# Kernel optimization log

Hardware: AMD Instinct MI355X
Metric: run time of the kernel (lower is better)

Reference implementation:

```python
import jax, jax.numpy as jnp
import numpy as np

B, T, M, H, E = 4, 2048, 1024, 16, 8
S = B * T              # total tokens
C = S // E             # deepspeed top-1 capacity, capacity_factor = 1.0
D = M // H             # head dim


def setup_inputs() -> dict:
    key = jax.random.key(0)
    ks = jax.random.split(key, 8)
    def nrm(k, shape, scale=0.02):
        return jax.random.normal(k, shape, jnp.float32) * scale
    return {
        "x": jax.random.normal(ks[0], (B, T, M), jnp.float32),
        "ln1_g": jnp.ones((M,), jnp.float32), "ln1_b": jnp.zeros((M,), jnp.float32),
        "in_proj_w": nrm(ks[1], (3 * M, M)), "in_proj_b": jnp.zeros((3 * M,), jnp.float32),
        "out_proj_w": nrm(ks[2], (M, M)), "out_proj_b": jnp.zeros((M,), jnp.float32),
        "ln2_g": jnp.ones((M,), jnp.float32), "ln2_b": jnp.zeros((M,), jnp.float32),
        "wg": nrm(ks[3], (M, E)),
        "w1": nrm(ks[4], (E, M, 4 * M)), "b1": jnp.zeros((E, 4 * M), jnp.float32),
        "w2": nrm(ks[5], (E, 4 * M, M)), "b2": jnp.zeros((E, M), jnp.float32),
    }


def layernorm(x, g, b):
    mu = x.mean(-1, keepdims=True)
    var = x.var(-1, keepdims=True)
    return (x - mu) * jax.lax.rsqrt(var + 1e-5) * g + b


def reference(x, ln1_g, ln1_b, in_proj_w, in_proj_b, out_proj_w, out_proj_b,
              ln2_g, ln2_b, wg, w1, b1, w2, b2):
    # --- pre-norm causal self-attention (nn.MultiheadAttention, batch_first) ---
    h = layernorm(x, ln1_g, ln1_b)
    qkv = h @ in_proj_w.T + in_proj_b                 # [B,T,3M]
    q, k, v = jnp.split(qkv, 3, axis=-1)
    split_heads = lambda t: t.reshape(B, T, H, D).transpose(0, 2, 1, 3)
    q, k, v = split_heads(q), split_heads(k), split_heads(v)
    scores = jnp.einsum('bhqd,bhkd->bhqk', q, k) / np.float32(np.sqrt(D))
    causal = jnp.tril(jnp.ones((T, T), bool))
    scores = jnp.where(causal, scores, jnp.float32(-jnp.inf))
    attn = jax.nn.softmax(scores, axis=-1)
    o = jnp.einsum('bhqk,bhkd->bhqd', attn, v).transpose(0, 2, 1, 3).reshape(B, T, M)
    x = x + o @ out_proj_w.T + out_proj_b

    # --- pre-norm top-1 MoE FFN (deepspeed-style dispatch with capacity drop) ---
    h = layernorm(x, ln2_g, ln2_b)
    flat = h.reshape(S, M)
    gates = jax.nn.softmax(flat @ wg, axis=-1)        # [S,E]
    idx = jnp.argmax(gates, axis=-1)                  # top-1 expert per token
    onehot = jax.nn.one_hot(idx, E, dtype=flat.dtype) # [S,E]
    # position of each token within its expert's queue
    pos = jnp.take_along_axis(jnp.cumsum(onehot, 0) - 1.0, idx[:, None], 1)[:, 0].astype(jnp.int32)
    keep = (pos < C).astype(flat.dtype)               # capacity drop
    pos_c = jnp.clip(pos, 0, C - 1)
    gate_val = jnp.take_along_axis(gates, idx[:, None], 1)[:, 0] * keep
    # scatter-dispatch tokens -> [E,C,M]
    disp = jnp.zeros((E, C, M), flat.dtype).at[idx, pos_c].add(flat * keep[:, None])
    # per-expert grouped GEMM FFN: M -> 4M -> M with exact GELU
    h1 = jax.nn.gelu(jnp.einsum('ecm,emf->ecf', disp, w1) + b1[:, None, :], approximate=False)
    eo = jnp.einsum('ecf,efm->ecm', h1, w2) + b2[:, None, :]
    # gather-combine, weight by gate prob (dropped tokens get zero)
    moe = eo[idx, pos_c] * gate_val[:, None]
    return x + moe.reshape(B, T, M)
```

## Files before the change

kernel.cpp:

```cpp
#include <hip/hip_runtime.h>
#include <hip/hip_bf16.h>
#include <math.h>

#define B_ 4
#define T_ 2048
#define M_ 1024
#define H_ 16
#define E_ 8
#define S_ (B_*T_)
#define C_ (S_/E_)
#define D_ (M_/H_)
#define F_ (4*M_)

typedef unsigned short ushort_t;
typedef __attribute__((ext_vector_type(8))) short bf16x8;
typedef __attribute__((ext_vector_type(4))) float f32x4;

__device__ __forceinline__ float gelu_exact(float x) {
    return 0.5f * x * (1.0f + erff(x * 0.70710678118654752440f));
}

__device__ __forceinline__ unsigned short f2bf(float f) {
    unsigned int u = __float_as_uint(f);
    u = (u + 0x7FFFu + ((u >> 16) & 1u)) >> 16;
    return (unsigned short)u;
}

__device__ __forceinline__ float bf2f(unsigned short h) {
    return __uint_as_float(((unsigned)h) << 16);
}

__device__ __forceinline__ void gload_lds16(const void* g, void* l) {
    __builtin_amdgcn_global_load_lds(
        (const __attribute__((address_space(1))) unsigned int*)g,
        (__attribute__((address_space(3))) unsigned int*)l,
        16, 0, 0);
}

__device__ __forceinline__ void lgkm0() {
    asm volatile("s_waitcnt lgkmcnt(0)" ::: "memory");
}

__global__ __launch_bounds__(256) void ln_kernel(const float* __restrict__ x,
                                                 const float* __restrict__ g,
                                                 const float* __restrict__ bta,
                                                 float* __restrict__ out)
{
    const int row = blockIdx.x;
    const int tid = threadIdx.x;
    const float4 v = reinterpret_cast<const float4*>(x + (size_t)row * M_)[tid];
    float s = v.x + v.y + v.z + v.w;
    __shared__ float red[4];
    #pragma unroll
    for (int off = 32; off > 0; off >>= 1) s += __shfl_down(s, off);
    if ((tid & 63) == 0) red[tid >> 6] = s;
    __syncthreads();
    const float mu = (red[0] + red[1] + red[2] + red[3]) * (1.0f / (float)M_);
    __syncthreads();
    float4 d;
    d.x = v.x - mu; d.y = v.y - mu; d.z = v.z - mu; d.w = v.w - mu;
    float q = d.x*d.x + d.y*d.y + d.z*d.z + d.w*d.w;
    #pragma unroll
    for (int off = 32; off > 0; off >>= 1) q += __shfl_down(q, off);
    if ((tid & 63) == 0) red[tid >> 6] = q;
    __syncthreads();
    const float var  = (red[0] + red[1] + red[2] + red[3]) * (1.0f / (float)M_);
    const float rstd = 1.0f / sqrtf(var + 1e-5f);
    const float4 gv = reinterpret_cast<const float4*>(g)[tid];
    const float4 bv = reinterpret_cast<const float4*>(bta)[tid];
    float4 o;
    o.x = d.x * rstd * gv.x + bv.x;
    o.y = d.y * rstd * gv.y + bv.y;
    o.z = d.z * rstd * gv.z + bv.z;
    o.w = d.w * rstd * gv.w + bv.w;
    reinterpret_cast<float4*>(out + (size_t)row * M_)[tid] = o;
}

__global__ __launch_bounds__(256) void ln_split_kernel(const float* __restrict__ x,
                                                       const float* __restrict__ g,
                                                       const float* __restrict__ bta,
                                                       ushort_t* __restrict__ hi,
                                                       ushort_t* __restrict__ lo)
{
    const int row = blockIdx.x;
    const int tid = threadIdx.x;
    const float4 v = reinterpret_cast<const float4*>(x + (size_t)row * M_)[tid];
    float s = v.x + v.y + v.z + v.w;
    __shared__ float red[4];
    #pragma unroll
    for (int off = 32; off > 0; off >>= 1) s += __shfl_down(s, off);
    if ((tid & 63) == 0) red[tid >> 6] = s;
    __syncthreads();
    const float mu = (red[0] + red[1] + red[2] + red[3]) * (1.0f / (float)M_);
    __syncthreads();
    float4 d;
    d.x = v.x - mu; d.y = v.y - mu; d.z = v.z - mu; d.w = v.w - mu;
    float q = d.x*d.x + d.y*d.y + d.z*d.z + d.w*d.w;
    #pragma unroll
    for (int off = 32; off > 0; off >>= 1) q += __shfl_down(q, off);
    if ((tid & 63) == 0) red[tid >> 6] = q;
    __syncthreads();
    const float var  = (red[0] + red[1] + red[2] + red[3]) * (1.0f / (float)M_);
    const float rstd = 1.0f / sqrtf(var + 1e-5f);
    const float4 gv = reinterpret_cast<const float4*>(g)[tid];
    const float4 bv = reinterpret_cast<const float4*>(bta)[tid];
    float o[4];
    o[0] = d.x * rstd * gv.x + bv.x;
    o[1] = d.y * rstd * gv.y + bv.y;
    o[2] = d.z * rstd * gv.z + bv.z;
    o[3] = d.w * rstd * gv.w + bv.w;
    ushort4 hh, ll;
    hh.x = f2bf(o[0]); ll.x = f2bf(o[0] - bf2f(hh.x));
    hh.y = f2bf(o[1]); ll.y = f2bf(o[1] - bf2f(hh.y));
    hh.z = f2bf(o[2]); ll.z = f2bf(o[2] - bf2f(hh.z));
    hh.w = f2bf(o[3]); ll.w = f2bf(o[3] - bf2f(hh.w));
    reinterpret_cast<ushort4*>(hi + (size_t)row * M_)[tid] = hh;
    reinterpret_cast<ushort4*>(lo + (size_t)row * M_)[tid] = ll;
}

__global__ __launch_bounds__(256) void split_kernel(const float* __restrict__ in,
                                                    ushort_t* __restrict__ hi,
                                                    ushort_t* __restrict__ lo,
                                                    int n4)
{
    const int i = blockIdx.x * 256 + threadIdx.x;
    if (i >= n4) return;
    const float4 v = reinterpret_cast<const float4*>(in)[i];
    ushort4 hh, ll;
    hh.x = f2bf(v.x); ll.x = f2bf(v.x - bf2f(hh.x));
    hh.y = f2bf(v.y); ll.y = f2bf(v.y - bf2f(hh.y));
    hh.z = f2bf(v.z); ll.z = f2bf(v.z - bf2f(hh.z));
    hh.w = f2bf(v.w); ll.w = f2bf(v.w - bf2f(hh.w));
    reinterpret_cast<ushort4*>(hi)[i] = hh;
    reinterpret_cast<ushort4*>(lo)[i] = ll;
}

__global__ __launch_bounds__(256) void vtrans_kernel(const ushort_t* __restrict__ qkvh,
                                                     const ushort_t* __restrict__ qkvl,
                                                     ushort_t* __restrict__ vth,
                                                     ushort_t* __restrict__ vtl)
{
    __shared__ ushort_t tile[64][72];
    const int t0 = blockIdx.x * 64, h = blockIdx.y, b = blockIdx.z;
    const int tid = threadIdx.x;
    const int tr = tid & 63, dc = (tid >> 6) * 16;
    const size_t src = ((size_t)(b*T_ + t0 + tr)) * (3*M_) + 2*M_ + h*64 + dc;
    const int dr = tid & 63, tc = (tid >> 6) * 16;
    const size_t dst = ((size_t)((b*H_ + h)*64 + dr)) * T_ + t0 + tc;

    #pragma unroll
    for (int pass = 0; pass < 2; ++pass) {
        const ushort_t* in = pass ? qkvl : qkvh;
        ushort_t* outp     = pass ? vtl  : vth;
        *reinterpret_cast<bf16x8*>(&tile[tr][dc])     = *reinterpret_cast<const bf16x8*>(in + src);
        *reinterpret_cast<bf16x8*>(&tile[tr][dc + 8]) = *reinterpret_cast<const bf16x8*>(in + src + 8);
        __syncthreads();
        bf16x8 o0, o1;
        #pragma unroll
        for (int j = 0; j < 8; ++j) {
            o0[j] = (short)tile[tc + j][dr];
            o1[j] = (short)tile[tc + 8 + j][dr];
        }
        *reinterpret_cast<bf16x8*>(outp + dst)     = o0;
        *reinterpret_cast<bf16x8*>(outp + dst + 8) = o1;
        __syncthreads();
    }
}

template<int EPI>
__global__ __launch_bounds__(256) void gemm_bf16x3(
    const ushort_t* __restrict__ Ahi, const ushort_t* __restrict__ Alo,
    const ushort_t* __restrict__ Bhi, const ushort_t* __restrict__ Blo,
    const float* __restrict__ bias, const float* __restrict__ res,
    void* __restrict__ C0, ushort_t* __restrict__ C1, int N, int K)
{
    __shared__ ushort_t AsH[128*32], AsL[128*32];
    __shared__ ushort_t BsH[128*32], BsL[128*32];

    const int t  = threadIdx.x;
    const int l  = t & 63;
    const int wv = t >> 6;
    const int wm = (wv & 1) * 64, wn = (wv >> 1) * 64;
    const int fr = l & 15, fk = (l >> 4) * 8;
    const int m0 = blockIdx.y * 128, n0 = blockIdx.x * 128;

    const size_t arow = (size_t)(m0 + (t >> 2)) * K + (t & 3) * 8;
    const size_t brow = (size_t)(n0 + (t >> 2)) * K + (t & 3) * 8;
    ushort_t* lAH = AsH + wv * 512;
    ushort_t* lAL = AsL + wv * 512;
    ushort_t* lBH = BsH + wv * 512;
    ushort_t* lBL = BsL + wv * 512;

    f32x4 acc[4][4] = {};

    for (int k0 = 0; k0 < K; k0 += 32) {
        __syncthreads();
        gload_lds16(Ahi + arow + k0, lAH);
        gload_lds16(Ahi + arow + k0 + (size_t)64 * K, lAH + 2048);
        gload_lds16(Alo + arow + k0, lAL);
        gload_lds16(Alo + arow + k0 + (size_t)64 * K, lAL + 2048);
        gload_lds16(Bhi + brow + k0, lBH);
        gload_lds16(Bhi + brow + k0 + (size_t)64 * K, lBH + 2048);
        gload_lds16(Blo + brow + k0, lBL);
        gload_lds16(Blo + brow + k0 + (size_t)64 * K, lBL + 2048);
        __syncthreads();
        bf16x8 ah[4], al[4], bh[4], bl[4];
        #pragma unroll
        for (int i = 0; i < 4; ++i) {
            ah[i] = *reinterpret_cast<const bf16x8*>(&AsH[(wm + i*16 + fr) * 32 + fk]);
            al[i] = *reinterpret_cast<const bf16x8*>(&AsL[(wm + i*16 + fr) * 32 + fk]);
            bh[i] = *reinterpret_cast<const bf16x8*>(&BsH[(wn + i*16 + fr) * 32 + fk]);
            bl[i] = *reinterpret_cast<const bf16x8*>(&BsL[(wn + i*16 + fr) * 32 + fk]);
        }
        #pragma unroll
        for (int mi = 0; mi < 4; ++mi) {
            #pragma unroll
            for (int ni = 0; ni < 4; ++ni) {
                acc[mi][ni] = __builtin_amdgcn_mfma_f32_16x16x32_bf16(ah[mi], bh[ni], acc[mi][ni], 0, 0, 0);
                acc[mi][ni] = __builtin_amdgcn_mfma_f32_16x16x32_bf16(al[mi], bh[ni], acc[mi][ni], 0, 0, 0);
                acc[mi][ni] = __builtin_amdgcn_mfma_f32_16x16x32_bf16(ah[mi], bl[ni], acc[mi][ni], 0, 0, 0);
            }
        }
    }

    const int l4 = (l >> 4) * 4;
    #pragma unroll
    for (int mi = 0; mi < 4; ++mi) {
        #pragma unroll
        for (int i = 0; i < 4; ++i) {
            const int row = m0 + wm + mi*16 + l4 + i;
            #pragma unroll
            for (int ni = 0; ni < 4; ++ni) {
                const int col = n0 + wn + ni*16 + fr;
                float v = acc[mi][ni][i] + bias[col];
                if (EPI == 1) {
                    v += res[(size_t)row * N + col];
                    ((float*)C0)[(size_t)row * N + col] = v;
                } else {
                    const ushort_t hb = f2bf(v);
                    ((ushort_t*)C0)[(size_t)row * N + col] = hb;
                    C1[(size_t)row * N + col] = f2bf(v - bf2f(hb));
                }
            }
        }
    }
}

__global__ __launch_bounds__(256) void attn_mfma_kernel(
    const ushort_t* __restrict__ qkvh, const ushort_t* __restrict__ qkvl,
    const ushort_t* __restrict__ vth,  const ushort_t* __restrict__ vtl,
    ushort_t* __restrict__ ohi, ushort_t* __restrict__ olo)
{
    const int j = (int)blockIdx.x;
    const int t = threadIdx.x;
    const int w = t >> 6, l = t & 63;
    const int r = l & 15, g = l >> 4;

    __shared__ ushort_t Khi[64*64], Klo[64*64];
    __shared__ ushort_t Vhi[64*64], Vlo[64*64];

    ushort_t* Pwh = Khi + w * 1024;
    ushort_t* Pwl = Klo + w * 1024;

    const int items[2] = { j, 2047 - j };

    const int srow = w*8 + (l >> 3);
    const int scol = ((l & 7) ^ (l >> 3)) * 8;
    const int d0 = w * 512 + l * 8;

    for (int ii = 0; ii < 2; ++ii) {
        const int item = items[ii];
        const int qt  = 31 - (item >> 6);
        const int rem = item & 63;
        const int h = rem >> 2, b = rem & 3;
        const int q0 = qt * 64;
        const size_t rowbase = (size_t)b * T_;
        const int hoff = h * D_;

        bf16x8 qh[2], ql[2];
        {
            const size_t qrow = (rowbase + q0 + 16*w + r) * (size_t)(3*M_) + hoff;
            #pragma unroll
            for (int ks = 0; ks < 2; ++ks) {
                qh[ks] = *reinterpret_cast<const bf16x8*>(qkvh + qrow + 32*ks + 8*g);
                ql[ks] = *reinterpret_cast<const bf16x8*>(qkvl + qrow + 32*ks + 8*g);
            }
        }

        const size_t ksrc0 = (rowbase + srow) * (size_t)(3*M_) + hoff + M_ + scol;
        const size_t vsrc0 = ((size_t)((b*H_ + h)*64 + srow)) * T_ + scol;

        bf16x8 stg[8];
        __syncthreads();
        {
            const size_t kb = ksrc0, vb = vsrc0;
            const size_t kstep = (size_t)32 * (3*M_);
            stg[0] = *reinterpret_cast<const bf16x8*>(qkvh + kb);
            stg[1] = *reinterpret_cast<const bf16x8*>(qkvh + kb + kstep);
            stg[2] = *reinterpret_cast<const bf16x8*>(qkvl + kb);
            stg[3] = *reinterpret_cast<const bf16x8*>(qkvl + kb + kstep);
            stg[4] = *reinterpret_cast<const bf16x8*>(vth + vb);
            stg[5] = *reinterpret_cast<const bf16x8*>(vth + vb + 32*T_);
            stg[6] = *reinterpret_cast<const bf16x8*>(vtl + vb);
            stg[7] = *reinterpret_cast<const bf16x8*>(vtl + vb + 32*T_);
            *reinterpret_cast<bf16x8*>(&Khi[d0])        = stg[0];
            *reinterpret_cast<bf16x8*>(&Khi[d0 + 2048]) = stg[1];
            *reinterpret_cast<bf16x8*>(&Klo[d0])        = stg[2];
            *reinterpret_cast<bf16x8*>(&Klo[d0 + 2048]) = stg[3];
            *reinterpret_cast<bf16x8*>(&Vhi[d0])        = stg[4];
            *reinterpret_cast<bf16x8*>(&Vhi[d0 + 2048]) = stg[5];
            *reinterpret_cast<bf16x8*>(&Vlo[d0])        = stg[6];
            *reinterpret_cast<bf16x8*>(&Vlo[d0 + 2048]) = stg[7];
        }
        __syncthreads();

        f32x4 oa[4] = {};
        float mrow[4] = {-__builtin_inff(), -__builtin_inff(), -__builtin_inff(), -__builtin_inff()};
        float lrow[4] = {};

        for (int kt = 0; kt <= qt; ++kt) {
            f32x4 sa[4] = {};
            #pragma unroll
            for (int ks = 0; ks < 2; ++ks) {
                bf16x8 kh[4], kl[4];
                #pragma unroll
                for (int nf = 0; nf < 4; ++nf) {
                    const int row = 16*nf + r;
                    const unsigned boff = (unsigned)(row * 128)
                        + (((unsigned)(ks*64 + g*16)) ^ ((unsigned)((row & 7) << 4)));
                    kh[nf] = *reinterpret_cast<const bf16x8*>((const char*)Khi + boff);
                    kl[nf] = *reinterpret_cast<const bf16x8*>((const char*)Klo + boff);
                }
                #pragma unroll
                for (int nf = 0; nf < 4; ++nf) {
                    sa[nf] = __builtin_amdgcn_mfma_f32_16x16x32_bf16(qh[ks], kh[nf], sa[nf], 0, 0, 0);
                    sa[nf] = __builtin_amdgcn_mfma_f32_16x16x32_bf16(ql[ks], kh[nf], sa[nf], 0, 0, 0);
                    sa[nf] = __builtin_amdgcn_mfma_f32_16x16x32_bf16(qh[ks], kl[nf], sa[nf], 0, 0, 0);
                }
            }

            if (kt < qt) {
                const size_t kb = ksrc0 + (size_t)((kt+1)*64) * (3*M_);
                const size_t vb = vsrc0 + (size_t)((kt+1)*64);
                const size_t kstep = (size_t)32 * (3*M_);
                stg[0] = *reinterpret_cast<const bf16x8*>(qkvh + kb);
                stg[1] = *reinterpret_cast<const bf16x8*>(qkvh + kb + kstep);
                stg[2] = *reinterpret_cast<const bf16x8*>(qkvl + kb);
                stg[3] = *reinterpret_cast<const bf16x8*>(qkvl + kb + kstep);
                stg[4] = *reinterpret_cast<const bf16x8*>(vth + vb);
                stg[5] = *reinterpret_cast<const bf16x8*>(vth + vb + 32*T_);
                stg[6] = *reinterpret_cast<const bf16x8*>(vtl + vb);
                stg[7] = *reinterpret_cast<const bf16x8*>(vtl + vb + 32*T_);
            }

            float sv[4][4];
            #pragma unroll
            for (int nf = 0; nf < 4; ++nf)
                #pragma unroll
                for (int i = 0; i < 4; ++i)
                    sv[nf][i] = sa[nf][i] * 0.125f;
            if (kt == qt) {
                #pragma unroll
                for (int nf = 0; nf < 4; ++nf) {
                    const int kvg = kt*64 + 16*nf + r;
                    #pragma unroll
                    for (int i = 0; i < 4; ++i) {
                        const int qg = q0 + 16*w + 4*g + i;
                        if (kvg > qg) sv[nf][i] = -3.0e38f;
                    }
                }
            }

            float tmax[4];
            #pragma unroll
            for (int i = 0; i < 4; ++i)
                tmax[i] = fmaxf(fmaxf(sv[0][i], sv[1][i]), fmaxf(sv[2][i], sv[3][i]));
            #pragma unroll
            for (int off = 1; off < 16; off <<= 1)
                #pragma unroll
                for (int i = 0; i < 4; ++i)
                    tmax[i] = fmaxf(tmax[i], __shfl_xor(tmax[i], off));
            float mnew[4], corr[4];
            #pragma unroll
            for (int i = 0; i < 4; ++i) {
                mnew[i] = fmaxf(mrow[i], tmax[i]);
                corr[i] = __expf(mrow[i] - mnew[i]);
            }
            float p[4][4];
            float rsum[4] = {};
            #pragma unroll
            for (int nf = 0; nf < 4; ++nf)
                #pragma unroll
                for (int i = 0; i < 4; ++i) {
                    p[nf][i] = __expf(sv[nf][i] - mnew[i]);
                    rsum[i] += p[nf][i];
                }
            #pragma unroll
            for (int off = 1; off < 16; off <<= 1)
                #pragma unroll
                for (int i = 0; i < 4; ++i)
                    rsum[i] += __shfl_xor(rsum[i], off);
            #pragma unroll
            for (int i = 0; i < 4; ++i) {
                lrow[i] = lrow[i] * corr[i] + rsum[i];
                mrow[i] = mnew[i];
            }
            #pragma unroll
            for (int df = 0; df < 4; ++df)
                #pragma unroll
                for (int i = 0; i < 4; ++i)
                    oa[df][i] *= corr[i];

            __syncthreads();

            #pragma unroll
            for (int nf = 0; nf < 4; ++nf) {
                #pragma unroll
                for (int i = 0; i < 4; ++i) {
                    const int q = 4*g + i;
                    const int kv = (16*nf + r) ^ ((q & 7) << 3);
                    const ushort_t phb = f2bf(p[nf][i]);
                    Pwh[q * 64 + kv] = phb;
                    Pwl[q * 64 + kv] = f2bf(p[nf][i] - bf2f(phb));
                }
            }
            lgkm0();

            #pragma unroll
            for (int ks = 0; ks < 2; ++ks) {
                const unsigned poff = (unsigned)(r * 64 + ((32*ks + 8*g) ^ ((r & 7) << 3)));
                const bf16x8 ph = *reinterpret_cast<const bf16x8*>(&Pwh[poff]);
                const bf16x8 pl = *reinterpret_cast<const bf16x8*>(&Pwl[poff]);
                #pragma unroll
                for (int df = 0; df < 4; ++df) {
                    const int vrow = 16*df + r;
                    const unsigned voff = (unsigned)(vrow * 128)
                        + (((unsigned)(ks*64 + g*16)) ^ ((unsigned)((vrow & 7) << 4)));
                    const bf16x8 vhf = *reinterpret_cast<const bf16x8*>((const char*)Vhi + voff);
                    const bf16x8 vlf = *reinterpret_cast<const bf16x8*>((const char*)Vlo + voff);
                    oa[df] = __builtin_amdgcn_mfma_f32_16x16x32_bf16(ph, vhf, oa[df], 0, 0, 0);
                    oa[df] = __builtin_amdgcn_mfma_f32_16x16x32_bf16(pl, vhf, oa[df], 0, 0, 0);
                    oa[df] = __builtin_amdgcn_mfma_f32_16x16x32_bf16(ph, vlf, oa[df], 0, 0, 0);
                }
            }

            if (kt < qt) {
                __syncthreads();
                *reinterpret_cast<bf16x8*>(&Khi[d0])        = stg[0];
                *reinterpret_cast<bf16x8*>(&Khi[d0 + 2048]) = stg[1];
                *reinterpret_cast<bf16x8*>(&Klo[d0])        = stg[2];
                *reinterpret_cast<bf16x8*>(&Klo[d0 + 2048]) = stg[3];
                *reinterpret_cast<bf16x8*>(&Vhi[d0])        = stg[4];
                *reinterpret_cast<bf16x8*>(&Vhi[d0 + 2048]) = stg[5];
                *reinterpret_cast<bf16x8*>(&Vlo[d0])        = stg[6];
                *reinterpret_cast<bf16x8*>(&Vlo[d0 + 2048]) = stg[7];
                __syncthreads();
            }
        }

        #pragma unroll
        for (int i = 0; i < 4; ++i) {
            const float inv = 1.0f / lrow[i];
            const size_t row = (rowbase + q0 + 16*w + 4*g + i) * (size_t)M_ + hoff;
            #pragma unroll
            for (int df = 0; df < 4; ++df) {
                const float v = oa[df][i] * inv;
                const ushort_t hb = f2bf(v);
                ohi[row + 16*df + r] = hb;
                olo[row + 16*df + r] = f2bf(v - bf2f(hb));
            }
        }
    }
}

__global__ __launch_bounds__(256) void gate_kernel(const float* __restrict__ h2,
                                                   const float* __restrict__ wg,
                                                   int* __restrict__ gidx,
                                                   float* __restrict__ gtop)
{
    const int s = blockIdx.x;
    const int e = threadIdx.x >> 5;
    const int l = threadIdx.x & 31;
    const float* row = h2 + (size_t)s * M_;
    float acc = 0.0f;
    for (int m = l; m < M_; m += 32) acc = fmaf(row[m], wg[m * E_ + e], acc);
    #pragma unroll
    for (int off = 16; off > 0; off >>= 1) acc += __shfl_down(acc, off, 32);
    __shared__ float lg[E_];
    if (l == 0) lg[e] = acc;
    __syncthreads();
    if (threadIdx.x == 0) {
        float mx = lg[0]; int bi = 0;
        #pragma unroll
        for (int i = 1; i < E_; ++i) { if (lg[i] > mx) { mx = lg[i]; bi = i; } }
        float den = 0.0f;
        #pragma unroll
        for (int i = 0; i < E_; ++i) den += expf(lg[i] - mx);
        gidx[s] = bi;
        gtop[s] = 1.0f / den;
    }
}

__global__ __launch_bounds__(1024) void scan_kernel(const int* __restrict__ gidx,
                                                    const float* __restrict__ gtop,
                                                    float* __restrict__ gate_val,
                                                    int* __restrict__ token_at)
{
    __shared__ int hist[1024][E_];
    const int tid = threadIdx.x;
    for (int i = tid; i < E_ * C_; i += 1024) token_at[i] = -1;
    int my[8];
    #pragma unroll
    for (int t = 0; t < 8; ++t) my[t] = gidx[tid * 8 + t];
    #pragma unroll
    for (int e = 0; e < E_; ++e) {
        int c = 0;
        #pragma unroll
        for (int t = 0; t < 8; ++t) c += (my[t] == e) ? 1 : 0;
        hist[tid][e] = c;
    }
    __syncthreads();
    if (tid < E_) {
        int run = 0;
        for (int t = 0; t < 1024; ++t) {
            const int v = hist[t][tid];
            hist[t][tid] = run;
            run += v;
        }
    }
    __syncthreads();
    #pragma unroll
    for (int t = 0; t < 8; ++t) {
        const int s = tid * 8 + t;
        const int e = my[t];
        const int p = hist[tid][e];
        hist[tid][e] = p + 1;
        const bool keep = (p < C_);
        gate_val[s] = keep ? gtop[s] : 0.0f;
        if (keep) token_at[e * C_ + p] = s;
    }
}

__global__ __launch_bounds__(256) void dispatch_bf16_kernel(const float* __restrict__ h2,
                                                            const int* __restrict__ token_at,
                                                            ushort_t* __restrict__ disp)
{
    const int ec = blockIdx.x;
    const int s = token_at[ec];
    ushort4* dst = reinterpret_cast<ushort4*>(disp + (size_t)ec * M_);
    if (s >= 0) {
        const float4 v = reinterpret_cast<const float4*>(h2 + (size_t)s * M_)[threadIdx.x];
        dst[threadIdx.x] = make_ushort4(f2bf(v.x), f2bf(v.y), f2bf(v.z), f2bf(v.w));
    } else {
        dst[threadIdx.x] = make_ushort4(0, 0, 0, 0);
    }
}

__global__ __launch_bounds__(256) void transpose_bf16_kernel(const float* __restrict__ in,
                                                             ushort_t* __restrict__ outp,
                                                             int R, int Cc)
{
    __shared__ float tile[32][33];
    const int e = blockIdx.z;
    in   += (size_t)e * R * Cc;
    outp += (size_t)e * R * Cc;
    const int tx = threadIdx.x & 31, ty0 = threadIdx.x >> 5;
    const int c0 = blockIdx.x * 32, r0 = blockIdx.y * 32;
    #pragma unroll
    for (int i = 0; i < 4; ++i)
        tile[ty0 + 8*i][tx] = in[(size_t)(r0 + ty0 + 8*i) * Cc + c0 + tx];
    __syncthreads();
    #pragma unroll
    for (int i = 0; i < 4; ++i)
        outp[(size_t)(c0 + ty0 + 8*i) * R + r0 + tx] = f2bf(tile[tx][ty0 + 8*i]);
}

template<int EPI>
__global__ __launch_bounds__(256) void gemm_mfma(
    const ushort_t* __restrict__ A, const ushort_t* __restrict__ Bt,
    const float* __restrict__ bias,
    const int* __restrict__ token_at, const float* __restrict__ gate_val,
    void* __restrict__ Cout, int N, int K,
    long strA, long strB, long strBias, long strC)
{
    const int e = blockIdx.z;
    A    += (size_t)e * (size_t)strA;
    Bt   += (size_t)e * (size_t)strB;
    bias += (size_t)e * (size_t)strBias;

    __shared__ ushort_t As[128 * 32];
    __shared__ ushort_t Bs[128 * 32];

    const int t  = threadIdx.x;
    const int l  = t & 63;
    const int wv = t >> 6;
    const int wm = (wv & 1) * 64, wn = (wv >> 1) * 64;
    const int fr = l & 15, fk = (l >> 4) * 8;
    const int m0 = blockIdx.y * 128, n0 = blockIdx.x * 128;

    const ushort_t* gA = A + (size_t)(m0 + (t >> 2)) * K + (t & 3) * 8;
    const ushort_t* gB = Bt + (size_t)(n0 + (t >> 2)) * K + (t & 3) * 8;
    ushort_t* lA = As + wv * 512;
    ushort_t* lB = Bs + wv * 512;

    f32x4 acc[4][4] = {};

    for (int k0 = 0; k0 < K; k0 += 32) {
        __syncthreads();
        gload_lds16(gA + k0, lA);
        gload_lds16(gA + k0 + (size_t)64 * K, lA + 2048);
        gload_lds16(gB + k0, lB);
        gload_lds16(gB + k0 + (size_t)64 * K, lB + 2048);
        __syncthreads();
        bf16x8 af[4], bfr[4];
        #pragma unroll
        for (int i = 0; i < 4; ++i)
            af[i] = *reinterpret_cast<const bf16x8*>(&As[(wm + i*16 + fr) * 32 + fk]);
        #pragma unroll
        for (int i = 0; i < 4; ++i)
            bfr[i] = *reinterpret_cast<const bf16x8*>(&Bs[(wn + i*16 + fr) * 32 + fk]);
        #pragma unroll
        for (int mi = 0; mi < 4; ++mi) {
            #pragma unroll
            for (int ni = 0; ni < 4; ++ni)
                acc[mi][ni] = __builtin_amdgcn_mfma_f32_16x16x32_bf16(
                    af[mi], bfr[ni], acc[mi][ni], 0, 0, 0);
        }
    }

    const int l4 = (l >> 4) * 4;
    if (EPI == 0) {
        ushort_t* Cc = (ushort_t*)Cout + (size_t)e * (size_t)strC;
        #pragma unroll
        for (int ni = 0; ni < 4; ++ni) {
            const int cl = n0 + wn + ni*16 + fr;
            const float bb = bias[cl];
            #pragma unroll
            for (int mi = 0; mi < 4; ++mi) {
                #pragma unroll
                for (int i = 0; i < 4; ++i) {
                    const int rr = m0 + wm + mi*16 + l4 + i;
                    Cc[(size_t)rr * N + cl] = f2bf(gelu_exact(acc[mi][ni][i] + bb));
                }
            }
        }
    } else {
        float* Co = (float*)Cout;
        const int* ta = token_at + e * C_;
        #pragma unroll
        for (int mi = 0; mi < 4; ++mi) {
            #pragma unroll
            for (int i = 0; i < 4; ++i) {
                const int rr = m0 + wm + mi*16 + l4 + i;
                const int s = ta[rr];
                if (s >= 0) {
                    const float gvl = gate_val[s];
                    #pragma unroll
                    for (int ni = 0; ni < 4; ++ni) {
                        const int cl = n0 + wn + ni*16 + fr;
                        Co[(size_t)s * N + cl] += gvl * (acc[mi][ni][i] + bias[cl]);
                    }
                }
            }
        }
    }
}

extern "C" void kernel_launch(void* const* d_in, const int* in_sizes, int n_in,
                              void* d_out, int out_size, void* d_ws, size_t ws_size,
                              hipStream_t stream)
{
    const float* x    = (const float*)d_in[0];
    const float* ln1g = (const float*)d_in[1];
    const float* ln1b = (const float*)d_in[2];
    const float* Wqkv = (const float*)d_in[3];
    const float* bqkv = (const float*)d_in[4];
    const float* Wout = (const float*)d_in[5];
    const float* bout = (const float*)d_in[6];
    const float* ln2g = (const float*)d_in[7];
    const float* ln2b = (const float*)d_in[8];
    const float* wg   = (const float*)d_in[9];
    const float* w1   = (const float*)d_in[10];
    const float* b1   = (const float*)d_in[11];
    const float* w2   = (const float*)d_in[12];
    const float* b2   = (const float*)d_in[13];
    float* out = (float*)d_out;

    char* ws = (char*)d_ws;
    ushort_t* ahi   = (ushort_t*)ws;
    ushort_t* alo   = (ushort_t*)(ws + ((size_t)16  << 20));
    float*    buf_h = (float*)ws;
    ushort_t* qkvh  = (ushort_t*)(ws + ((size_t)32  << 20));
    ushort_t* qkvl  = (ushort_t*)(ws + ((size_t)80  << 20));
    ushort_t* vth   = (ushort_t*)(ws + ((size_t)128 << 20));
    ushort_t* vtl   = (ushort_t*)(ws + ((size_t)144 << 20));
    ushort_t* ohi   = (ushort_t*)(ws + ((size_t)160 << 20));
    ushort_t* olo   = (ushort_t*)(ws + ((size_t)176 << 20));
    ushort_t* wqh   = (ushort_t*)(ws + ((size_t)128 << 20));
    ushort_t* wql   = (ushort_t*)(ws + ((size_t)134 << 20));
    ushort_t* woh   = (ushort_t*)(ws + ((size_t)192 << 20));
    ushort_t* wol   = (ushort_t*)(ws + ((size_t)194 << 20));
    ushort_t* w1t   = (ushort_t*)(ws + ((size_t)32  << 20));
    ushort_t* w2t   = (ushort_t*)(ws + ((size_t)32  << 20));
    ushort_t* dispb = (ushort_t*)(ws + ((size_t)96  << 20));
    ushort_t* h1b   = (ushort_t*)(ws + ((size_t)112 << 20));
    float*    buf_gtop = (float*)(ws + ((size_t)196 << 20));
    float*    buf_gv   = buf_gtop + S_;
    int*      buf_idx  = (int*)(buf_gv + S_);
    int*      buf_ta   = buf_idx + S_;

    split_kernel<<<(3*M_*M_/4 + 255)/256, 256, 0, stream>>>(Wqkv, wqh, wql, 3*M_*M_/4);
    split_kernel<<<(M_*M_/4 + 255)/256, 256, 0, stream>>>(Wout, woh, wol, M_*M_/4);
    ln_split_kernel<<<S_, 256, 0, stream>>>(x, ln1g, ln1b, ahi, alo);
    gemm_bf16x3<2><<<dim3(3*M_/128, S_/128, 1), 256, 0, stream>>>(
        ahi, alo, wqh, wql, bqkv, nullptr, qkvh, qkvl, 3*M_, M_);
    vtrans_kernel<<<dim3(T_/64, H_, B_), 256, 0, stream>>>(qkvh, qkvl, vth, vtl);
    attn_mfma_kernel<<<dim3(1024, 1, 1), 256, 0, stream>>>(qkvh, qkvl, vth, vtl, ohi, olo);
    gemm_bf16x3<1><<<dim3(M_/128, S_/128, 1), 256, 0, stream>>>(
        ohi, olo, woh, wol, bout, x, out, nullptr, M_, M_);

    ln_kernel<<<S_, 256, 0, stream>>>(out, ln2g, ln2b, buf_h);
    gate_kernel<<<S_, 256, 0, stream>>>(buf_h, wg, buf_idx, buf_gtop);
    scan_kernel<<<1, 1024, 0, stream>>>(buf_idx, buf_gtop, buf_gv, buf_ta);
    dispatch_bf16_kernel<<<E_*C_, 256, 0, stream>>>(buf_h, buf_ta, dispb);

    transpose_bf16_kernel<<<dim3(F_/32, M_/32, E_), 256, 0, stream>>>(w1, w1t, M_, F_);
    gemm_mfma<0><<<dim3(F_/128, C_/128, E_), 256, 0, stream>>>(
        dispb, w1t, b1, nullptr, nullptr, h1b, F_, M_,
        (long)C_*M_, (long)F_*M_, (long)F_, (long)C_*F_);
    transpose_bf16_kernel<<<dim3(M_/32, F_/32, E_), 256, 0, stream>>>(w2, w2t, F_, M_);
    gemm_mfma<1><<<dim3(M_/128, C_/128, E_), 256, 0, stream>>>(
        h1b, w2t, b2, buf_ta, buf_gv, out, M_, F_,
        (long)C_*F_, (long)M_*F_, (long)M_, 0);
}
```

Before: 981.8 us.

## Fuse LN2 with gating, prefetch K/V before QK MFMAs, skip unneeded rescale

```diff
diff --git a/kernel.cpp b/kernel.cpp
--- a/kernel.cpp
+++ b/kernel.cpp
@@ -39,41 +39,6 @@
 
 __device__ __forceinline__ void lgkm0() {
     asm volatile("s_waitcnt lgkmcnt(0)" ::: "memory");
-}
-
-__global__ __launch_bounds__(256) void ln_kernel(const float* __restrict__ x,
-                                                 const float* __restrict__ g,
-                                                 const float* __restrict__ bta,
-                                                 float* __restrict__ out)
-{
-    const int row = blockIdx.x;
-    const int tid = threadIdx.x;
-    const float4 v = reinterpret_cast<const float4*>(x + (size_t)row * M_)[tid];
-    float s = v.x + v.y + v.z + v.w;
-    __shared__ float red[4];
-    #pragma unroll
-    for (int off = 32; off > 0; off >>= 1) s += __shfl_down(s, off);
-    if ((tid & 63) == 0) red[tid >> 6] = s;
-    __syncthreads();
-    const float mu = (red[0] + red[1] + red[2] + red[3]) * (1.0f / (float)M_);
-    __syncthreads();
-    float4 d;
-    d.x = v.x - mu; d.y = v.y - mu; d.z = v.z - mu; d.w = v.w - mu;
-    float q = d.x*d.x + d.y*d.y + d.z*d.z + d.w*d.w;
-    #pragma unroll
-    for (int off = 32; off > 0; off >>= 1) q += __shfl_down(q, off);
-    if ((tid & 63) == 0) red[tid >> 6] = q;
-    __syncthreads();
-    const float var  = (red[0] + red[1] + red[2] + red[3]) * (1.0f / (float)M_);
-    const float rstd = 1.0f / sqrtf(var + 1e-5f);
-    const float4 gv = reinterpret_cast<const float4*>(g)[tid];
-    const float4 bv = reinterpret_cast<const float4*>(bta)[tid];
-    float4 o;
-    o.x = d.x * rstd * gv.x + bv.x;
-    o.y = d.y * rstd * gv.y + bv.y;
-    o.z = d.z * rstd * gv.z + bv.z;
-    o.w = d.w * rstd * gv.w + bv.w;
-    reinterpret_cast<float4*>(out + (size_t)row * M_)[tid] = o;
 }
 
 __global__ __launch_bounds__(256) void ln_split_kernel(const float* __restrict__ x,
@@ -116,6 +81,79 @@
     hh.w = f2bf(o[3]); ll.w = f2bf(o[3] - bf2f(hh.w));
     reinterpret_cast<ushort4*>(hi + (size_t)row * M_)[tid] = hh;
     reinterpret_cast<ushort4*>(lo + (size_t)row * M_)[tid] = ll;
+}
+
+__global__ __launch_bounds__(256) void ln_gate_kernel(const float* __restrict__ x,
+                                                      const float* __restrict__ g,
+                                                      const float* __restrict__ bta,
+                                                      const float* __restrict__ wg,
+                                                      float* __restrict__ h2,
+                                                      int* __restrict__ gidx,
+                                                      float* __restrict__ gtop)
+{
+    const int row = blockIdx.x;
+    const int tid = threadIdx.x;
+    const int wv = tid >> 6, ln = tid & 63;
+    const float4 v = reinterpret_cast<const float4*>(x + (size_t)row * M_)[tid];
+    float s = v.x + v.y + v.z + v.w;
+    __shared__ float red[4];
+    __shared__ float red2[4][E_];
+    #pragma unroll
+    for (int off = 32; off > 0; off >>= 1) s += __shfl_down(s, off);
+    if (ln == 0) red[wv] = s;
+    __syncthreads();
+    const float mu = (red[0] + red[1] + red[2] + red[3]) * (1.0f / (float)M_);
+    __syncthreads();
+    float4 d;
+    d.x = v.x - mu; d.y = v.y - mu; d.z = v.z - mu; d.w = v.w - mu;
+    float q = d.x*d.x + d.y*d.y + d.z*d.z + d.w*d.w;
+    #pragma unroll
+    for (int off = 32; off > 0; off >>= 1) q += __shfl_down(q, off);
+    if (ln == 0) red[wv] = q;
+    __syncthreads();
+    const float var  = (red[0] + red[1] + red[2] + red[3]) * (1.0f / (float)M_);
+    const float rstd = 1.0f / sqrtf(var + 1e-5f);
+    const float4 gv = reinterpret_cast<const float4*>(g)[tid];
+    const float4 bv = reinterpret_cast<const float4*>(bta)[tid];
+    float o[4];
+    o[0] = d.x * rstd * gv.x + bv.x;
+    o[1] = d.y * rstd * gv.y + bv.y;
+    o[2] = d.z * rstd * gv.z + bv.z;
+    o[3] = d.w * rstd * gv.w + bv.w;
+    reinterpret_cast<float4*>(h2 + (size_t)row * M_)[tid] = make_float4(o[0], o[1], o[2], o[3]);
+
+    float part[E_] = {};
+    #pragma unroll
+    for (int j = 0; j < 4; ++j) {
+        const float4 w0 = reinterpret_cast<const float4*>(wg)[(4*tid + j) * 2];
+        const float4 w1 = reinterpret_cast<const float4*>(wg)[(4*tid + j) * 2 + 1];
+        part[0] = fmaf(o[j], w0.x, part[0]); part[1] = fmaf(o[j], w0.y, part[1]);
+        part[2] = fmaf(o[j], w0.z, part[2]); part[3] = fmaf(o[j], w0.w, part[3]);
+        part[4] = fmaf(o[j], w1.x, part[4]); part[5] = fmaf(o[j], w1.y, part[5]);
+        part[6] = fmaf(o[j], w1.z, part[6]); part[7] = fmaf(o[j], w1.w, part[7]);
+    }
+    #pragma unroll
+    for (int off = 32; off > 0; off >>= 1)
+        #pragma unroll
+        for (int e = 0; e < E_; ++e) part[e] += __shfl_down(part[e], off);
+    if (ln == 0)
+        #pragma unroll
+        for (int e = 0; e < E_; ++e) red2[wv][e] = part[e];
+    __syncthreads();
+    if (tid == 0) {
+        float lg[E_];
+        #pragma unroll
+        for (int e = 0; e < E_; ++e)
+            lg[e] = red2[0][e] + red2[1][e] + red2[2][e] + red2[3][e];
+        float mx = lg[0]; int bi = 0;
+        #pragma unroll
+        for (int i = 1; i < E_; ++i) { if (lg[i] > mx) { mx = lg[i]; bi = i; } }
+        float den = 0.0f;
+        #pragma unroll
+        for (int i = 0; i < E_; ++i) den += expf(lg[i] - mx);
+        gidx[row] = bi;
+        gtop[row] = 1.0f / den;
+    }
 }
 
 __global__ __launch_bounds__(256) void split_kernel(const float* __restrict__ in,
@@ -319,26 +357,6 @@
         float lrow[4] = {};
 
         for (int kt = 0; kt <= qt; ++kt) {
-            f32x4 sa[4] = {};
-            #pragma unroll
-            for (int ks = 0; ks < 2; ++ks) {
-                bf16x8 kh[4], kl[4];
-                #pragma unroll
-                for (int nf = 0; nf < 4; ++nf) {
-                    const int row = 16*nf + r;
-                    const unsigned boff = (unsigned)(row * 128)
-                        + (((unsigned)(ks*64 + g*16)) ^ ((unsigned)((row & 7) << 4)));
-                    kh[nf] = *reinterpret_cast<const bf16x8*>((const char*)Khi + boff);
-                    kl[nf] = *reinterpret_cast<const bf16x8*>((const char*)Klo + boff);
-                }
-                #pragma unroll
-                for (int nf = 0; nf < 4; ++nf) {
-                    sa[nf] = __builtin_amdgcn_mfma_f32_16x16x32_bf16(qh[ks], kh[nf], sa[nf], 0, 0, 0);
-                    sa[nf] = __builtin_amdgcn_mfma_f32_16x16x32_bf16(ql[ks], kh[nf], sa[nf], 0, 0, 0);
-                    sa[nf] = __builtin_amdgcn_mfma_f32_16x16x32_bf16(qh[ks], kl[nf], sa[nf], 0, 0, 0);
-                }
-            }
-
             if (kt < qt) {
                 const size_t kb = ksrc0 + (size_t)((kt+1)*64) * (3*M_);
                 const size_t vb = vsrc0 + (size_t)((kt+1)*64);
@@ -353,6 +371,26 @@
                 stg[7] = *reinterpret_cast<const bf16x8*>(vtl + vb + 32*T_);
             }
 
+            f32x4 sa[4] = {};
+            #pragma unroll
+            for (int ks = 0; ks < 2; ++ks) {
+                bf16x8 kh[4], kl[4];
+                #pragma unroll
+                for (int nf = 0; nf < 4; ++nf) {
+                    const int row = 16*nf + r;
+                    const unsigned boff = (unsigned)(row * 128)
+                        + (((unsigned)(ks*64 + g*16)) ^ ((unsigned)((row & 7) << 4)));
+                    kh[nf] = *reinterpret_cast<const bf16x8*>((const char*)Khi + boff);
+                    kl[nf] = *reinterpret_cast<const bf16x8*>((const char*)Klo + boff);
+                }
+                #pragma unroll
+                for (int nf = 0; nf < 4; ++nf) {
+                    sa[nf] = __builtin_amdgcn_mfma_f32_16x16x32_bf16(qh[ks], kh[nf], sa[nf], 0, 0, 0);
+                    sa[nf] = __builtin_amdgcn_mfma_f32_16x16x32_bf16(ql[ks], kh[nf], sa[nf], 0, 0, 0);
+                    sa[nf] = __builtin_amdgcn_mfma_f32_16x16x32_bf16(qh[ks], kl[nf], sa[nf], 0, 0, 0);
+                }
+            }
+
             float sv[4][4];
             #pragma unroll
             for (int nf = 0; nf < 4; ++nf)
@@ -380,12 +418,14 @@
                 #pragma unroll
                 for (int i = 0; i < 4; ++i)
                     tmax[i] = fmaxf(tmax[i], __shfl_xor(tmax[i], off));
-            float mnew[4], corr[4];
+            float mnew[4];
+            bool grow = false;
             #pragma unroll
             for (int i = 0; i < 4; ++i) {
                 mnew[i] = fmaxf(mrow[i], tmax[i]);
-                corr[i] = __expf(mrow[i] - mnew[i]);
-            }
+                grow |= (tmax[i] > mrow[i]);
+            }
+            const bool need = __any(grow);
             float p[4][4];
             float rsum[4] = {};
             #pragma unroll
@@ -400,16 +440,24 @@
                 #pragma unroll
                 for (int i = 0; i < 4; ++i)
                     rsum[i] += __shfl_xor(rsum[i], off);
-            #pragma unroll
-            for (int i = 0; i < 4; ++i) {
-                lrow[i] = lrow[i] * corr[i] + rsum[i];
-                mrow[i] = mnew[i];
-            }
-            #pragma unroll
-            for (int df = 0; df < 4; ++df)
-                #pragma unroll
-                for (int i = 0; i < 4; ++i)
-                    oa[df][i] *= corr[i];
+            if (need) {
+                float corr[4];
+                #pragma unroll
+                for (int i = 0; i < 4; ++i) corr[i] = __expf(mrow[i] - mnew[i]);
+                #pragma unroll
+                for (int i = 0; i < 4; ++i) {
+                    lrow[i] = lrow[i] * corr[i] + rsum[i];
+                    mrow[i] = mnew[i];
+                }
+                #pragma unroll
+                for (int df = 0; df < 4; ++df)
+                    #pragma unroll
+                    for (int i = 0; i < 4; ++i)
+                        oa[df][i] *= corr[i];
+            } else {
+                #pragma unroll
+                for (int i = 0; i < 4; ++i) lrow[i] += rsum[i];
+            }
 
             __syncthreads();
 
@@ -417,11 +465,11 @@
             for (int nf = 0; nf < 4; ++nf) {
                 #pragma unroll
                 for (int i = 0; i < 4; ++i) {
-                    const int q = 4*g + i;
-                    const int kv = (16*nf + r) ^ ((q & 7) << 3);
+                    const int qq = 4*g + i;
+                    const int kv = (16*nf + r) ^ ((qq & 7) << 3);
                     const ushort_t phb = f2bf(p[nf][i]);
-                    Pwh[q * 64 + kv] = phb;
-                    Pwl[q * 64 + kv] = f2bf(p[nf][i] - bf2f(phb));
+                    Pwh[qq * 64 + kv] = phb;
+                    Pwl[qq * 64 + kv] = f2bf(p[nf][i] - bf2f(phb));
                 }
             }
             lgkm0();
@@ -470,34 +518,6 @@
                 olo[row + 16*df + r] = f2bf(v - bf2f(hb));
             }
         }
-    }
-}
-
-__global__ __launch_bounds__(256) void gate_kernel(const float* __restrict__ h2,
-                                                   const float* __restrict__ wg,
-                                                   int* __restrict__ gidx,
-                                                   float* __restrict__ gtop)
-{
-    const int s = blockIdx.x;
-    const int e = threadIdx.x >> 5;
-    const int l = threadIdx.x & 31;
-    const float* row = h2 + (size_t)s * M_;
-    float acc = 0.0f;
-    for (int m = l; m < M_; m += 32) acc = fmaf(row[m], wg[m * E_ + e], acc);
-    #pragma unroll
-    for (int off = 16; off > 0; off >>= 1) acc += __shfl_down(acc, off, 32);
-    __shared__ float lg[E_];
-    if (l == 0) lg[e] = acc;
-    __syncthreads();
-    if (threadIdx.x == 0) {
-        float mx = lg[0]; int bi = 0;
-        #pragma unroll
-        for (int i = 1; i < E_; ++i) { if (lg[i] > mx) { mx = lg[i]; bi = i; } }
-        float den = 0.0f;
-        #pragma unroll
-        for (int i = 0; i < E_; ++i) den += expf(lg[i] - mx);
-        gidx[s] = bi;
-        gtop[s] = 1.0f / den;
     }
 }
 
@@ -719,8 +739,7 @@
     gemm_bf16x3<1><<<dim3(M_/128, S_/128, 1), 256, 0, stream>>>(
         ohi, olo, woh, wol, bout, x, out, nullptr, M_, M_);
 
-    ln_kernel<<<S_, 256, 0, stream>>>(out, ln2g, ln2b, buf_h);
-    gate_kernel<<<S_, 256, 0, stream>>>(buf_h, wg, buf_idx, buf_gtop);
+    ln_gate_kernel<<<S_, 256, 0, stream>>>(out, ln2g, ln2b, wg, buf_h, buf_idx, buf_gtop);
     scan_kernel<<<1, 1024, 0, stream>>>(buf_idx, buf_gtop, buf_gv, buf_ta);
     dispatch_bf16_kernel<<<E_*C_, 256, 0, stream>>>(buf_h, buf_ta, dispb);
 
```

Measured after the change: 908.5 us. 7.5% less time.
